# Kernel optimization log

Measured on AMD Instinct MI355X. Metric: run time of the kernel, lower is better.

The kernel has to match this reference:

```python
import jax, jax.numpy as jnp
import numpy as np

B, S, H, L, NH, F, V, K, R = 64, 512, 256, 4, 8, 1024, 50265, 8, 25
DH = H // NH
EPS = 1e-5


def layernorm(x, g, b):
    mu = x.mean(-1, keepdims=True)
    var = ((x - mu) ** 2).mean(-1, keepdims=True)
    return (x - mu) * jax.lax.rsqrt(var + EPS) * g + b


def setup_inputs() -> dict:
    key = jax.random.key(0)
    ks = jax.random.split(key, 24)
    input_ids = jax.random.randint(ks[0], (B, S), 0, V, dtype=jnp.int64)
    # prefix attention mask with variable valid lengths (ragged sequences)
    lengths = jax.random.randint(ks[1], (B,), 16, S + 1)
    attention_mask = (jnp.arange(S)[None, :] < lengths[:, None]).astype(jnp.int32)
    sub_indices = jax.random.randint(ks[2], (B, K), 0, S, dtype=jnp.int64)
    obj_indices = jax.random.randint(ks[3], (B, K), 0, S, dtype=jnp.int64)
    sub_counts = jax.random.randint(ks[4], (B,), 0, K + 1, dtype=jnp.int32)
    obj_counts = jax.random.randint(ks[5], (B,), 0, K + 1, dtype=jnp.int32)
    sc = 0.02
    p = {
        'emb': jax.random.normal(ks[6], (V, H), jnp.float32) * sc,
        'Wqkv': jax.random.normal(ks[7], (L, H, 3 * H), jnp.float32) * sc,
        'bqkv': jnp.zeros((L, 3 * H), jnp.float32),
        'Wo': jax.random.normal(ks[8], (L, H, H), jnp.float32) * sc,
        'bo': jnp.zeros((L, H), jnp.float32),
        'ln1_g': jnp.ones((L, H), jnp.float32), 'ln1_b': jnp.zeros((L, H), jnp.float32),
        'ln2_g': jnp.ones((L, H), jnp.float32), 'ln2_b': jnp.zeros((L, H), jnp.float32),
        'W1': jax.random.normal(ks[9], (L, H, F), jnp.float32) * sc,
        'b1': jnp.zeros((L, F), jnp.float32),
        'W2': jax.random.normal(ks[10], (L, F, H), jnp.float32) * sc,
        'b2': jnp.zeros((L, H), jnp.float32),
        'lnf_g': jnp.ones((H,), jnp.float32), 'lnf_b': jnp.zeros((H,), jnp.float32),
        'mW1': jax.random.normal(ks[11], (3 * H, H), jnp.float32) * sc,
        'mb1': jnp.zeros((H,), jnp.float32),
        'mW2': jax.random.normal(ks[12], (H, R), jnp.float32) * sc,
        'mb2': jnp.zeros((R,), jnp.float32),
    }
    return dict(input_ids=input_ids, attention_mask=attention_mask,
                sub_indices=sub_indices, sub_counts=sub_counts,
                obj_indices=obj_indices, obj_counts=obj_counts, **p)


def _encoder(input_ids, attention_mask, emb, Wqkv, bqkv, Wo, bo,
             ln1_g, ln1_b, ln2_g, ln2_b, W1, b1, W2, b2, lnf_g, lnf_b):
    x = emb[input_ids]  # [B,S,H]
    kbias = jnp.where(attention_mask[:, None, None, :] > 0, 0.0, -1e9)  # mask keys
    scale = 1.0 / np.sqrt(DH)
    for l in range(L):  # small fixed layer loop
        qkv = x @ Wqkv[l] + bqkv[l]
        q, k, v = jnp.split(qkv, 3, axis=-1)
        q = q.reshape(B, S, NH, DH).transpose(0, 2, 1, 3)
        k = k.reshape(B, S, NH, DH).transpose(0, 2, 1, 3)
        v = v.reshape(B, S, NH, DH).transpose(0, 2, 1, 3)
        scores = jnp.einsum('bhqd,bhkd->bhqk', q, k) * scale + kbias
        attn = jax.nn.softmax(scores, axis=-1)
        o = jnp.einsum('bhqk,bhkd->bhqd', attn, v).transpose(0, 2, 1, 3).reshape(B, S, H)
        x = layernorm(x + o @ Wo[l] + bo[l], ln1_g[l], ln1_b[l])
        h = jax.nn.relu(x @ W1[l] + b1[l]) @ W2[l] + b2[l]
        x = layernorm(x + h, ln2_g[l], ln2_b[l])
    return layernorm(x, lnf_g, lnf_b)


def _pooled(seq, idx, counts):
    g = jnp.take_along_axis(seq, idx[:, :, None], axis=1)  # [B,K,H]
    m = (jnp.arange(K)[None, :] < counts[:, None]).astype(seq.dtype)
    s = (g * m[:, :, None]).sum(1)
    c = counts.astype(seq.dtype)[:, None]
    return jnp.where(c > 0, s / jnp.maximum(c, 1.0), 0.0)  # zeros if no indices


def reference(input_ids, attention_mask, sub_indices, sub_counts, obj_indices, obj_counts,
              emb, Wqkv, bqkv, Wo, bo, ln1_g, ln1_b, ln2_g, ln2_b,
              W1, b1, W2, b2, lnf_g, lnf_b, mW1, mb1, mW2, mb2):
    seq = _encoder(input_ids, attention_mask, emb, Wqkv, bqkv, Wo, bo,
                   ln1_g, ln1_b, ln2_g, ln2_b, W1, b1, W2, b2, lnf_g, lnf_b)
    sub = _pooled(seq, sub_indices, sub_counts)
    obj = _pooled(seq, obj_indices, obj_counts)
    mask = attention_mask.astype(seq.dtype)
    lens = mask.sum(1)[:, None]
    story = jnp.where(lens > 0, (seq * mask[:, :, None]).sum(1) / jnp.maximum(lens, 1.0),
                      seq.mean(1))
    feat = jnp.concatenate([sub, obj, story], axis=-1)  # [B,3H]
    logits = jax.nn.relu(feat @ mW1 + mb1) @ mW2 + mb2
    return logits
```

## Files before the change

kernel.cpp:

```cpp
#include <hip/hip_runtime.h>
#include <hip/hip_bf16.h>


typedef __hip_bfloat16 bf16;
typedef __attribute__((ext_vector_type(8))) short short8;
typedef __attribute__((ext_vector_type(4))) float f32x4;

#define S_LEN 512
#define H_DIM 256
#define NTOK  32768
#define QSCALE 0.25503488f

__device__ __forceinline__ void gload_lds16(const void* g, void* l) {
  __builtin_amdgcn_global_load_lds(
      (const __attribute__((address_space(1))) unsigned int*)g,
      (__attribute__((address_space(3))) unsigned int*)l, 16, 0, 0);
}

__device__ __forceinline__ unsigned short f2bu(float x) {
  bf16 t = __float2bfloat16(x);
  return *reinterpret_cast<unsigned short*>(&t);
}

__global__ __launch_bounds__(64) void lens_kernel(
    const int* __restrict__ amask, int* __restrict__ ntiles,
    int* __restrict__ lenb) {
  const int b = blockIdx.x, t = threadIdx.x;
  int c = 0;
#pragma unroll
  for (int i = 0; i < 8; ++i) c += amask[b * S_LEN + t + i * 64];
#pragma unroll
  for (int off = 1; off < 64; off <<= 1) c += __shfl_xor(c, off);
  if (t == 0) {
    lenb[b] = c;
    ntiles[b] = (c + 63) >> 6;
  }
}

__global__ __launch_bounds__(64) void order_kernel(
    const int* __restrict__ ntiles, int* __restrict__ ordb) {
  const int b = threadIdx.x;
  const int ntb = ntiles[b];
  int rank = 0;
  for (int j = 0; j < 64; ++j) {
    const int ntj = __shfl(ntb, j);
    rank += (ntj > ntb) || (ntj == ntb && j < b);
  }
  ordb[rank] = b;
}

__global__ __launch_bounds__(256) void tcast_kernel(
    const float* __restrict__ in, bf16* __restrict__ out, int K, int N) {
  const int l = blockIdx.z;
  in  += (size_t)l * K * N;
  out += (size_t)l * K * N;
  __shared__ float t[32][33];
  const int n0 = blockIdx.x * 32, k0 = blockIdx.y * 32;
  const int c = threadIdx.x & 31, r = threadIdx.x >> 5;
#pragma unroll
  for (int rr = r; rr < 32; rr += 8)
    t[rr][c] = in[(size_t)(k0 + rr) * N + n0 + c];
  __syncthreads();
#pragma unroll
  for (int rr = r; rr < 32; rr += 8)
    out[(size_t)(n0 + rr) * K + k0 + c] = __float2bfloat16(t[c][rr]);
}

__global__ __launch_bounds__(256) void embed_kernel(
    const int* __restrict__ ids, const float* __restrict__ emb,
    float* __restrict__ X, bf16* __restrict__ Xb) {
  size_t i4 = (size_t)blockIdx.x * 256 + threadIdx.x;
  int tok = (int)(i4 >> 6);
  int d4  = (int)(i4 & 63);
  float4 v = *(const float4*)&emb[(size_t)ids[tok] * H_DIM + d4 * 4];
  *(float4*)&X[i4 * 4] = v;
  ushort4 pk;
  pk.x = f2bu(v.x); pk.y = f2bu(v.y); pk.z = f2bu(v.z); pk.w = f2bu(v.w);
  *(ushort4*)&Xb[i4 * 4] = pk;
}

#define SRC_CHUNK(tid_) (((tid_) & 3) ^ (((tid_) >> 3) & 3))

template<int MODE, bool RELU>
__global__ __launch_bounds__(256) void hgemm_kernel(
    const bf16* __restrict__ A, const bf16* __restrict__ Bt,
    const float* __restrict__ bias, float* __restrict__ Cf,
    bf16* __restrict__ Cb, bf16* __restrict__ Vt,
    int M, int N, int K) {
  __shared__ __align__(16) bf16 Sh[16384];
  bf16* const As0 = Sh;
  bf16* const Bs0 = Sh + 8192;
  const int tid = threadIdx.x;
  const int wv = tid >> 6, ln = tid & 63;
  const int fr = ln & 15, g4 = ln >> 4;
  const int wr = wv >> 1, wc = wv & 1;
  const int m0 = blockIdx.x * 128, n0 = blockIdx.y * 128;
  const int lr = tid >> 2;
  const int lk = SRC_CHUNK(tid) * 8;
  const int rc = (g4 ^ ((fr >> 1) & 3)) * 8;

#define STAGE_G(buf, kk) do {                                                  \
    const int kof_ = (kk) * 32;                                                \
    gload_lds16(A  + (size_t)(m0 + lr) * K + kof_ + lk,                        \
                &As0[(buf) * 4096 + wv * 512]);                                \
    gload_lds16(A  + (size_t)(m0 + 64 + lr) * K + kof_ + lk,                   \
                &As0[(buf) * 4096 + 2048 + wv * 512]);                         \
    gload_lds16(Bt + (size_t)(n0 + lr) * K + kof_ + lk,                        \
                &Bs0[(buf) * 4096 + wv * 512]);                                \
    gload_lds16(Bt + (size_t)(n0 + 64 + lr) * K + kof_ + lk,                   \
                &Bs0[(buf) * 4096 + 2048 + wv * 512]);                         \
  } while (0)

  f32x4 acc[4][4];
#pragma unroll
  for (int i = 0; i < 4; ++i)
#pragma unroll
    for (int j = 0; j < 4; ++j)
      acc[i][j] = (f32x4){0.f, 0.f, 0.f, 0.f};

  const int NT = K >> 5;
  STAGE_G(0, 0);
  __syncthreads();
  int cur = 0;
  for (int kt = 0; kt < NT; ++kt) {
    if (kt + 1 < NT) STAGE_G(cur ^ 1, kt + 1);
    short8 af[4], bfv[4];
#pragma unroll
    for (int i = 0; i < 4; ++i)
      af[i] = *(const short8*)
          &As0[cur * 4096 + (wr * 64 + i * 16 + fr) * 32 + rc];
#pragma unroll
    for (int j = 0; j < 4; ++j)
      bfv[j] = *(const short8*)
          &Bs0[cur * 4096 + (wc * 64 + j * 16 + fr) * 32 + rc];
#pragma unroll
    for (int i = 0; i < 4; ++i)
#pragma unroll
      for (int j = 0; j < 4; ++j)
        acc[i][j] = __builtin_amdgcn_mfma_f32_16x16x32_bf16(
            af[i], bfv[j], acc[i][j], 0, 0, 0);
    __syncthreads();
    cur ^= 1;
  }
#undef STAGE_G

  const bool vpath = (MODE == 2) && (n0 >= 512);
#pragma unroll
  for (int j = 0; j < 4; ++j) {
    const int nl = wc * 64 + j * 16 + fr;
    const int n = n0 + nl;
    const float bv = bias[n];
    const float sc = (MODE == 2 && n < 256) ? QSCALE : 1.0f;
#pragma unroll
    for (int i = 0; i < 4; ++i) {
      const int mlb = wr * 64 + i * 16 + g4 * 4;
#pragma unroll
      for (int r = 0; r < 4; ++r) {
        float o = acc[i][j][r] + bv;
        if (RELU) o = fmaxf(o, 0.f);
        o *= sc;
        const int ml = mlb + r;
        const int addr = vpath ? nl * 128 + (ml ^ ((nl & 7) << 3))
                               : ml * 128 + (nl ^ ((ml & 7) << 3));
        Sh[addr] = __float2bfloat16(o);
      }
    }
  }
  __syncthreads();
  if (!vpath) {
    const int ldc = (MODE == 1) ? N : 768;
#pragma unroll
    for (int p = 0; p < 8; ++p) {
      const int cid = p * 256 + tid;
      const int ml = cid >> 4, mc = cid & 15;
      const short8 v =
          *(const short8*)&Sh[ml * 128 + ((mc * 8) ^ ((ml & 7) << 3))];
      *(short8*)&Cb[(size_t)(m0 + ml) * ldc + n0 + mc * 8] = v;
    }
  } else {
    const int bb = m0 >> 9;
#pragma unroll
    for (int p = 0; p < 8; ++p) {
      const int cid = p * 256 + tid;
      const int ddl = cid >> 4, mc = cid & 15;
      const short8 v =
          *(const short8*)&Sh[ddl * 128 + ((mc * 8) ^ ((ddl & 7) << 3))];
      const int dd = (n0 - 512) + ddl;
      const int hh = dd >> 5, ddd = dd & 31;
      const int s8 = (m0 & 511) + mc * 8;
      const int ssw = (s8 & ~63) | ((s8 & 63) ^ ((ddd & 7) << 3));
      *(short8*)&Vt[(((size_t)bb * 8 + hh) * 32 + ddd) * 512 + ssw] = v;
    }
  }
}

__global__ __launch_bounds__(256) void hgemm_ln_kernel(
    const bf16* __restrict__ A, const bf16* __restrict__ Bt,
    const float* __restrict__ bias, float* __restrict__ X,
    bf16* __restrict__ Xb, const float* __restrict__ g,
    const float* __restrict__ bt, int K) {
  __shared__ __align__(16) bf16 Sh[20480];
  bf16* const As0 = Sh;
  bf16* const Bs0 = Sh + 4096;
  float* const rsum = (float*)Sh;
  float* const rsq  = (float*)(Sh + 512);
  bf16*  const XbT  = Sh + 1024;
  float* const XfT  = (float*)(Sh + 1024);
  const int tid = threadIdx.x;
  const int wv = tid >> 6;
  const int ln = tid & 63;
  const int fr = ln & 15, g4 = ln >> 4;
  const int m0 = blockIdx.x * 64;
  const int rc = (g4 ^ ((fr >> 1) & 3)) * 8;

#define STAGE_L(buf, kk) do {                                                  \
    const int kof_ = (kk) * 32;                                                \
    gload_lds16(A + (size_t)(m0 + (tid >> 2)) * K + kof_ +                     \
                    SRC_CHUNK(tid) * 8,                                        \
                &As0[(buf) * 2048 + wv * 512]);                                \
    _Pragma("unroll")                                                          \
    for (int e = 0; e < 4; ++e) {                                              \
      const int vt = e * 256 + tid;                                            \
      gload_lds16(Bt + (size_t)(vt >> 2) * K + kof_ + SRC_CHUNK(vt) * 8,       \
                  &Bs0[(buf) * 8192 + e * 2048 + wv * 512]);                   \
    }                                                                          \
  } while (0)

  f32x4 acc[4][4];
#pragma unroll
  for (int i = 0; i < 4; ++i)
#pragma unroll
    for (int j = 0; j < 4; ++j)
      acc[i][j] = (f32x4){0.f, 0.f, 0.f, 0.f};

  const int NT = K >> 5;
  STAGE_L(0, 0);
  __syncthreads();
  int cur = 0;
  for (int kt = 0; kt < NT; ++kt) {
    if (kt + 1 < NT) STAGE_L(cur ^ 1, kt + 1);
    short8 af[4], bfv[4];
#pragma unroll
    for (int i = 0; i < 4; ++i)
      af[i] = *(const short8*)&As0[cur * 2048 + (i * 16 + fr) * 32 + rc];
#pragma unroll
    for (int j = 0; j < 4; ++j)
      bfv[j] = *(const short8*)
          &Bs0[cur * 8192 + (wv * 64 + j * 16 + fr) * 32 + rc];
#pragma unroll
    for (int i = 0; i < 4; ++i)
#pragma unroll
      for (int j = 0; j < 4; ++j)
        acc[i][j] = __builtin_amdgcn_mfma_f32_16x16x32_bf16(
            af[i], bfv[j], acc[i][j], 0, 0, 0);
    __syncthreads();
    cur ^= 1;
  }
#undef STAGE_L

  float gj[4], bj[4], bsj[4];
#pragma unroll
  for (int j = 0; j < 4; ++j) {
    const int n = wv * 64 + j * 16 + fr;
    gj[j] = g[n]; bj[j] = bt[n]; bsj[j] = bias[n];
  }
#pragma unroll
  for (int i = 0; i < 4; ++i) {
#pragma unroll
    for (int r = 0; r < 4; ++r) {
      const int m = m0 + i * 16 + g4 * 4 + r;
#pragma unroll
      for (int j = 0; j < 4; ++j)
        acc[i][j][r] += bsj[j] + X[(size_t)m * 256 + wv * 64 + j * 16 + fr];
    }
  }
#pragma unroll
  for (int i = 0; i < 4; ++i) {
#pragma unroll
    for (int r = 0; r < 4; ++r) {
      float sp = acc[i][0][r] + acc[i][1][r] + acc[i][2][r] + acc[i][3][r];
      float qp = acc[i][0][r] * acc[i][0][r] + acc[i][1][r] * acc[i][1][r] +
                 acc[i][2][r] * acc[i][2][r] + acc[i][3][r] * acc[i][3][r];
#pragma unroll
      for (int off = 1; off < 16; off <<= 1) {
        sp += __shfl_xor(sp, off);
        qp += __shfl_xor(qp, off);
      }
      if (fr == 0) {
        const int ri = i * 16 + g4 * 4 + r;
        rsum[wv * 64 + ri] = sp;
        rsq[wv * 64 + ri] = qp;
      }
    }
  }
  __syncthreads();
#pragma unroll
  for (int i = 0; i < 4; ++i) {
#pragma unroll
    for (int r = 0; r < 4; ++r) {
      const int ri = i * 16 + g4 * 4 + r;
      const float tot = rsum[ri] + rsum[64 + ri] + rsum[128 + ri] +
                        rsum[192 + ri];
      const float tq = rsq[ri] + rsq[64 + ri] + rsq[128 + ri] + rsq[192 + ri];
      const float mu = tot * (1.0f / 256.0f);
      const float var = tq * (1.0f / 256.0f) - mu * mu;
      const float rstd = rsqrtf(var + 1e-5f);
#pragma unroll
      for (int j = 0; j < 4; ++j)
        acc[i][j][r] = (acc[i][j][r] - mu) * rstd * gj[j] + bj[j];
    }
  }
  __syncthreads();
#pragma unroll
  for (int i = 0; i < 4; ++i)
#pragma unroll
    for (int r = 0; r < 4; ++r) {
      const int ml = i * 16 + g4 * 4 + r;
#pragma unroll
      for (int j = 0; j < 4; ++j) {
        const int nl = wv * 64 + j * 16 + fr;
        XbT[ml * 256 + (nl ^ ((ml & 7) << 3))] = __float2bfloat16(acc[i][j][r]);
      }
    }
  __syncthreads();
#pragma unroll
  for (int p = 0; p < 8; ++p) {
    const int c8 = p * 256 + tid;
    const int row = c8 >> 5, cc = c8 & 31;
    const short8 v =
        *(const short8*)&XbT[row * 256 + ((cc * 8) ^ ((row & 7) << 3))];
    *(short8*)&Xb[(size_t)(m0 + row) * 256 + cc * 8] = v;
  }
#pragma unroll
  for (int pass = 0; pass < 2; ++pass) {
    __syncthreads();
    if ((wv >> 1) == pass) {
      const int cbase = (wv & 1) * 64;
#pragma unroll
      for (int i = 0; i < 4; ++i)
#pragma unroll
        for (int r = 0; r < 4; ++r) {
          const int ml = i * 16 + g4 * 4 + r;
#pragma unroll
          for (int j = 0; j < 4; ++j) {
            const int c = cbase + j * 16 + fr;
            XfT[ml * 128 + (c ^ ((ml & 7) << 2))] = acc[i][j][r];
          }
        }
    }
    __syncthreads();
#pragma unroll
    for (int p = 0; p < 8; ++p) {
      const int c4 = p * 256 + tid;
      const int row = c4 >> 5, cc = c4 & 31;
      const float4 v = *(const float4*)
          &XfT[row * 128 + ((cc * 4) ^ ((row & 7) << 2))];
      *(float4*)&X[(size_t)(m0 + row) * 256 + pass * 128 + cc * 4] = v;
    }
  }
}

__global__ __launch_bounds__(256) void attn_mfma_kernel(
    const bf16* __restrict__ QKVb, const bf16* __restrict__ Vt,
    const int* __restrict__ amask, const int* __restrict__ ntiles,
    const int* __restrict__ ordb, bf16* __restrict__ Ob) {
  const int b = ordb[blockIdx.z];
  const int h = blockIdx.y, q0 = blockIdx.x * 64;
  const int tid = threadIdx.x;
  const int wv = tid >> 6, ln = tid & 63;
  const int fr = ln & 15, g4 = ln >> 4;
  const int f8 = (fr & 7) << 3;
  const int rc = (g4 ^ ((fr >> 1) & 3)) * 8;
  const int bh32 = (b * 8 + h) * 32;
  __shared__ __align__(16) bf16 Ks[2][2048];
  __shared__ __align__(16) bf16 Vs[2][2048];
  __shared__ __align__(16) bf16 Ps[4096];
  __shared__ __align__(16) float Ms[64];

  const int nt = ntiles[b];

#define STAGE_A(buf, kt_) do {                                                 \
    const int k0_ = (kt_) * 64;                                                \
    gload_lds16(QKVb + (size_t)(b * S_LEN + k0_ + (tid >> 2)) * 768 + 256 +    \
                    h * 32 + SRC_CHUNK(tid) * 8,                               \
                &Ks[(buf)][wv * 512]);                                         \
    gload_lds16(Vt + (size_t)(bh32 + (tid >> 3)) * 512 + k0_ + (tid & 7) * 8,  \
                &Vs[(buf)][wv * 512]);                                         \
    if ((kt_) == nt - 1 && tid < 64)                                           \
      Ms[tid] = (amask[b * S_LEN + k0_ + tid] != 0) ? 0.f : -1e9f;             \
  } while (0)

  gload_lds16(QKVb + (size_t)(b * S_LEN + q0 + (tid >> 2)) * 768 + h * 32 +
                  SRC_CHUNK(tid) * 8,
              &Ps[wv * 512]);
  STAGE_A(0, 0);
  __syncthreads();
  const short8 qb = *(const short8*)&Ps[(wv * 16 + fr) * 32 + rc];
  __syncthreads();

  f32x4 accO[2];
  accO[0] = (f32x4){0.f, 0.f, 0.f, 0.f};
  accO[1] = (f32x4){0.f, 0.f, 0.f, 0.f};
  float mrun = -1e30f, lrun = 0.f;
  const int srcq = 20 * g4;

  int cur = 0;
  for (int kt = 0; kt < nt; ++kt) {
    if (kt + 1 < nt) STAGE_A(cur ^ 1, kt + 1);
    const bool bnd = (kt == nt - 1);

    f32x4 st[4];
#pragma unroll
    for (int kb = 0; kb < 4; ++kb) {
      const short8 kf = *(const short8*)&Ks[cur][(kb * 16 + fr) * 32 + rc];
      f32x4 z = (f32x4){0.f, 0.f, 0.f, 0.f};
      st[kb] = __builtin_amdgcn_mfma_f32_16x16x32_bf16(kf, qb, z, 0, 0, 0);
    }

    float p[16];
    if (bnd) {
#pragma unroll
      for (int kb = 0; kb < 4; ++kb) {
        const f32x4 mv = ((const f32x4*)Ms)[kb * 4 + g4];
#pragma unroll
        for (int rr = 0; rr < 4; ++rr) p[kb * 4 + rr] = st[kb][rr] + mv[rr];
      }
    } else {
#pragma unroll
      for (int kb = 0; kb < 4; ++kb)
#pragma unroll
        for (int rr = 0; rr < 4; ++rr) p[kb * 4 + rr] = st[kb][rr];
    }

    const float a0 = fmaxf(fmaxf(p[0], p[1]), p[2]);
    const float a1 = fmaxf(fmaxf(p[3], p[4]), p[5]);
    const float a2 = fmaxf(fmaxf(p[6], p[7]), p[8]);
    const float a3 = fmaxf(fmaxf(p[9], p[10]), p[11]);
    const float a4 = fmaxf(fmaxf(p[12], p[13]), p[14]);
    float mx = fmaxf(fmaxf(fmaxf(a0, a1), fmaxf(a2, a3)), fmaxf(a4, p[15]));
    mx = fmaxf(mx, __shfl_xor(mx, 16));
    mx = fmaxf(mx, __shfl_xor(mx, 32));

    float corr = 1.f;
    if (!__all(mx <= mrun + 8.f)) {
      const float mnew = fmaxf(mrun, mx);
      corr = exp2f(mrun - mnew);
      mrun = mnew;
#pragma unroll
      for (int rr = 0; rr < 4; ++rr) {
        const float cs = __shfl(corr, srcq + rr);
        accO[0][rr] *= cs;
        accO[1][rr] *= cs;
      }
    }

#pragma unroll
    for (int i = 0; i < 16; ++i) p[i] = exp2f(p[i] - mrun);
    const float b0 = p[0] + p[1], b1 = p[2] + p[3], b2 = p[4] + p[5],
                b3 = p[6] + p[7], b4 = p[8] + p[9], b5 = p[10] + p[11],
                b6 = p[12] + p[13], b7 = p[14] + p[15];
    float ps = ((b0 + b1) + (b2 + b3)) + ((b4 + b5) + (b6 + b7));
    ps += __shfl_xor(ps, 16);
    ps += __shfl_xor(ps, 32);
    lrun = lrun * corr + ps;

#pragma unroll
    for (int kb = 0; kb < 4; ++kb) {
      ushort4 w4;
      w4.x = f2bu(p[kb * 4 + 0]);
      w4.y = f2bu(p[kb * 4 + 1]);
      w4.z = f2bu(p[kb * 4 + 2]);
      w4.w = f2bu(p[kb * 4 + 3]);
      *(ushort4*)&Ps[wv * 1024 + fr * 64 + ((kb * 16 + g4 * 4) ^ f8)] = w4;
    }

#pragma unroll
    for (int kk = 0; kk < 2; ++kk) {
      const short8 pa = *(const short8*)
          &Ps[wv * 1024 + fr * 64 + ((kk * 32 + g4 * 8) ^ f8)];
#pragma unroll
      for (int df = 0; df < 2; ++df) {
        const short8 vb = *(const short8*)
            &Vs[cur][(df * 16 + fr) * 64 + ((kk * 32 + g4 * 8) ^ f8)];
        accO[df] = __builtin_amdgcn_mfma_f32_16x16x32_bf16(
            pa, vb, accO[df], 0, 0, 0);
      }
    }
    __syncthreads();
    cur ^= 1;
  }
#undef STAGE_A

  const float inv = 1.0f / lrun;
#pragma unroll
  for (int rr = 0; rr < 4; ++rr) {
    const float iv = __shfl(inv, srcq + rr);
    const int q = q0 + wv * 16 + g4 * 4 + rr;
    const size_t orow = ((size_t)b * S_LEN + q) * H_DIM + h * 32;
    Ob[orow + fr]      = __float2bfloat16(accO[0][rr] * iv);
    Ob[orow + 16 + fr] = __float2bfloat16(accO[1][rr] * iv);
  }
}

__global__ __launch_bounds__(256) void lnf_pool_kernel(
    float* __restrict__ X, const float* __restrict__ g,
    const float* __restrict__ bt, const int* __restrict__ amask,
    float* __restrict__ Pstory) {
  const int b = blockIdx.x, sg = blockIdx.y;
  const int tid = threadIdx.x, wv = tid >> 6, ln = tid & 63;
  const float4 gg = ((const float4*)g)[ln];
  const float4 bb = ((const float4*)bt)[ln];
  float ax = 0.f, ay = 0.f, az = 0.f, aw = 0.f;
  for (int t = wv; t < 64; t += 4) {
    const size_t tok = (size_t)b * S_LEN + sg * 64 + t;
    float4 v = ((const float4*)X)[tok * 64 + ln];
    float s = v.x + v.y + v.z + v.w;
#pragma unroll
    for (int off = 1; off < 64; off <<= 1) s += __shfl_xor(s, off);
    const float mu = s * (1.0f / 256.0f);
    const float dx = v.x - mu, dy = v.y - mu, dz = v.z - mu, dw = v.w - mu;
    float sq = dx * dx + dy * dy + dz * dz + dw * dw;
#pragma unroll
    for (int off = 1; off < 64; off <<= 1) sq += __shfl_xor(sq, off);
    const float rstd = rsqrtf(sq * (1.0f / 256.0f) + 1e-5f);
    float4 o;
    o.x = dx * rstd * gg.x + bb.x;
    o.y = dy * rstd * gg.y + bb.y;
    o.z = dz * rstd * gg.z + bb.z;
    o.w = dw * rstd * gg.w + bb.w;
    ((float4*)X)[tok * 64 + ln] = o;
    if (amask[tok]) { ax += o.x; ay += o.y; az += o.z; aw += o.w; }
  }
  __shared__ float part[4][256];
  part[wv][ln * 4 + 0] = ax;
  part[wv][ln * 4 + 1] = ay;
  part[wv][ln * 4 + 2] = az;
  part[wv][ln * 4 + 3] = aw;
  __syncthreads();
  const float tot = part[0][tid] + part[1][tid] + part[2][tid] + part[3][tid];
  Pstory[((size_t)b * 8 + sg) * 256 + tid] = tot;
}

__global__ __launch_bounds__(256) void poolcls_kernel(
    const float* __restrict__ X, const float* __restrict__ Pstory,
    const int* __restrict__ lenb,
    const int* __restrict__ sub_idx, const int* __restrict__ sub_cnt,
    const int* __restrict__ obj_idx, const int* __restrict__ obj_cnt,
    const float* __restrict__ mW1, const float* __restrict__ mb1,
    const float* __restrict__ mW2, const float* __restrict__ mb2,
    float* __restrict__ out) {
  const int b = blockIdx.x, t = threadIdx.x;
  __shared__ float fs[768];
  __shared__ float hid[256];
  const float* xb = X + (size_t)b * S_LEN * H_DIM;
  {
    float s = 0.f;
#pragma unroll
    for (int i = 0; i < 8; ++i) s += Pstory[((size_t)b * 8 + i) * 256 + t];
    fs[512 + t] = s / (float)lenb[b];
  }
  {
    const int cc = sub_cnt[b];
    float s2 = 0.f;
    for (int j = 0; j < cc; ++j)
      s2 += xb[(size_t)sub_idx[b * 8 + j] * H_DIM + t];
    fs[t] = (cc > 0) ? s2 / (float)cc : 0.f;
  }
  {
    const int cc = obj_cnt[b];
    float s2 = 0.f;
    for (int j = 0; j < cc; ++j)
      s2 += xb[(size_t)obj_idx[b * 8 + j] * H_DIM + t];
    fs[256 + t] = (cc > 0) ? s2 / (float)cc : 0.f;
  }
  __syncthreads();
  float acc = mb1[t];
  for (int k = 0; k < 768; ++k) acc += fs[k] * mW1[(size_t)k * 256 + t];
  hid[t] = fmaxf(acc, 0.f);
  __syncthreads();
  if (t < 25) {
    float o = mb2[t];
    for (int j = 0; j < 256; ++j) o += hid[j] * mW2[j * 25 + t];
    out[b * 25 + t] = o;
  }
}

extern "C" void kernel_launch(void* const* d_in, const int* in_sizes, int n_in,
                              void* d_out, int out_size, void* d_ws, size_t ws_size,
                              hipStream_t stream) {
  const int*   input_ids = (const int*)d_in[0];
  const int*   amask     = (const int*)d_in[1];
  const int*   sub_idx   = (const int*)d_in[2];
  const int*   sub_cnt   = (const int*)d_in[3];
  const int*   obj_idx   = (const int*)d_in[4];
  const int*   obj_cnt   = (const int*)d_in[5];
  const float* emb  = (const float*)d_in[6];
  const float* Wqkv = (const float*)d_in[7];
  const float* bqkv = (const float*)d_in[8];
  const float* Wo   = (const float*)d_in[9];
  const float* bo   = (const float*)d_in[10];
  const float* ln1g = (const float*)d_in[11];
  const float* ln1b = (const float*)d_in[12];
  const float* ln2g = (const float*)d_in[13];
  const float* ln2b = (const float*)d_in[14];
  const float* W1   = (const float*)d_in[15];
  const float* b1   = (const float*)d_in[16];
  const float* W2   = (const float*)d_in[17];
  const float* b2   = (const float*)d_in[18];
  const float* lnfg = (const float*)d_in[19];
  const float* lnfb = (const float*)d_in[20];
  const float* mW1  = (const float*)d_in[21];
  const float* mb1  = (const float*)d_in[22];
  const float* mW2  = (const float*)d_in[23];
  const float* mb2  = (const float*)d_in[24];
  float* out = (float*)d_out;

  char* w = (char*)d_ws;
  float* X    = (float*)w;                         w += (size_t)NTOK * 256 * 4;
  bf16*  Xb   = (bf16*)w;                          w += (size_t)NTOK * 256 * 2;
  bf16*  QKVb = (bf16*)w;                          w += (size_t)NTOK * 768 * 2;
  bf16*  Vtg  = (bf16*)w;                          w += (size_t)NTOK * 256 * 2;
  bf16*  Ob   = (bf16*)w;                          w += (size_t)NTOK * 256 * 2;
  bf16*  Wqkvt= (bf16*)w;                          w += (size_t)4 * 768 * 256 * 2;
  bf16*  Wot  = (bf16*)w;                          w += (size_t)4 * 256 * 256 * 2;
  bf16*  W1t  = (bf16*)w;                          w += (size_t)4 * 1024 * 256 * 2;
  bf16*  W2t  = (bf16*)w;                          w += (size_t)4 * 256 * 1024 * 2;
  float* Pstory = (float*)w;                       w += (size_t)64 * 8 * 256 * 4;
  int*   ntiles = (int*)w;                         w += 256;
  int*   lenb   = (int*)w;                         w += 256;
  int*   ordb   = (int*)w;                         w += 256;
  bf16*  Hb   = QKVb;

  lens_kernel<<<64, 64, 0, stream>>>(amask, ntiles, lenb);
  order_kernel<<<1, 64, 0, stream>>>(ntiles, ordb);
  tcast_kernel<<<dim3(24, 8, 4), 256, 0, stream>>>(Wqkv, Wqkvt, 256, 768);
  tcast_kernel<<<dim3(8, 8, 4), 256, 0, stream>>>(Wo, Wot, 256, 256);
  tcast_kernel<<<dim3(32, 8, 4), 256, 0, stream>>>(W1, W1t, 256, 1024);
  tcast_kernel<<<dim3(8, 32, 4), 256, 0, stream>>>(W2, W2t, 1024, 256);

  embed_kernel<<<8192, 256, 0, stream>>>(input_ids, emb, X, Xb);

  for (int l = 0; l < 4; ++l) {
    const bf16* Wqkvt_l = Wqkvt + (size_t)l * 768 * 256;
    const bf16* Wot_l   = Wot + (size_t)l * 256 * 256;
    const bf16* W1t_l   = W1t + (size_t)l * 1024 * 256;
    const bf16* W2t_l   = W2t + (size_t)l * 256 * 1024;

    hgemm_kernel<2, false><<<dim3(256, 6), 256, 0, stream>>>(
        Xb, Wqkvt_l, bqkv + (size_t)l * 768, nullptr, QKVb, Vtg, NTOK, 768, 256);
    attn_mfma_kernel<<<dim3(8, 8, 64), 256, 0, stream>>>(
        QKVb, Vtg, amask, ntiles, ordb, Ob);
    hgemm_ln_kernel<<<512, 256, 0, stream>>>(
        Ob, Wot_l, bo + (size_t)l * 256, X, Xb,
        ln1g + l * 256, ln1b + l * 256, 256);
    hgemm_kernel<1, true><<<dim3(256, 8), 256, 0, stream>>>(
        Xb, W1t_l, b1 + (size_t)l * 1024, nullptr, Hb, nullptr, NTOK, 1024, 256);
    hgemm_ln_kernel<<<512, 256, 0, stream>>>(
        Hb, W2t_l, b2 + (size_t)l * 256, X, Xb,
        ln2g + l * 256, ln2b + l * 256, 1024);
  }
  lnf_pool_kernel<<<dim3(64, 8), 256, 0, stream>>>(X, lnfg, lnfb, amask, Pstory);
  poolcls_kernel<<<64, 256, 0, stream>>>(X, Pstory, lenb, sub_idx, sub_cnt,
                                         obj_idx, obj_cnt, mW1, mb1, mW2, mb2,
                                         out);
}
```

Measured before the change: 730.0 us.

## Keep residual stream in bf16 only and compute softmax row sums via MFMA

```diff
diff --git a/kernel.cpp b/kernel.cpp
--- a/kernel.cpp
+++ b/kernel.cpp
@@ -20,6 +20,10 @@
 __device__ __forceinline__ unsigned short f2bu(float x) {
   bf16 t = __float2bfloat16(x);
   return *reinterpret_cast<unsigned short*>(&t);
+}
+__device__ __forceinline__ float bu2f(unsigned short u) {
+  unsigned int x = (unsigned int)u << 16;
+  return __uint_as_float(x);
 }
 
 __global__ __launch_bounds__(64) void lens_kernel(
@@ -68,12 +72,11 @@
 
 __global__ __launch_bounds__(256) void embed_kernel(
     const int* __restrict__ ids, const float* __restrict__ emb,
-    float* __restrict__ X, bf16* __restrict__ Xb) {
+    bf16* __restrict__ Xb) {
   size_t i4 = (size_t)blockIdx.x * 256 + threadIdx.x;
   int tok = (int)(i4 >> 6);
   int d4  = (int)(i4 & 63);
   float4 v = *(const float4*)&emb[(size_t)ids[tok] * H_DIM + d4 * 4];
-  *(float4*)&X[i4 * 4] = v;
   ushort4 pk;
   pk.x = f2bu(v.x); pk.y = f2bu(v.y); pk.z = f2bu(v.z); pk.w = f2bu(v.w);
   *(ushort4*)&Xb[i4 * 4] = pk;
@@ -196,16 +199,14 @@
 
 __global__ __launch_bounds__(256) void hgemm_ln_kernel(
     const bf16* __restrict__ A, const bf16* __restrict__ Bt,
-    const float* __restrict__ bias, float* __restrict__ X,
-    bf16* __restrict__ Xb, const float* __restrict__ g,
-    const float* __restrict__ bt, int K) {
+    const float* __restrict__ bias, bf16* __restrict__ Xbf,
+    const float* __restrict__ g, const float* __restrict__ bt, int K) {
   __shared__ __align__(16) bf16 Sh[20480];
   bf16* const As0 = Sh;
   bf16* const Bs0 = Sh + 4096;
   float* const rsum = (float*)Sh;
   float* const rsq  = (float*)(Sh + 512);
   bf16*  const XbT  = Sh + 1024;
-  float* const XfT  = (float*)(Sh + 1024);
   const int tid = threadIdx.x;
   const int wv = tid >> 6;
   const int ln = tid & 63;
@@ -258,6 +259,15 @@
   }
 #undef STAGE_L
 
+#pragma unroll
+  for (int p = 0; p < 8; ++p) {
+    const int seg = p * 4 + wv;
+    gload_lds16(Xbf + (size_t)(m0 + seg * 2 + (ln >> 5)) * 256 +
+                    (ln & 31) * 8,
+                &XbT[seg * 512]);
+  }
+  __syncthreads();
+
   float gj[4], bj[4], bsj[4];
 #pragma unroll
   for (int j = 0; j < 4; ++j) {
@@ -268,10 +278,13 @@
   for (int i = 0; i < 4; ++i) {
 #pragma unroll
     for (int r = 0; r < 4; ++r) {
-      const int m = m0 + i * 16 + g4 * 4 + r;
-#pragma unroll
-      for (int j = 0; j < 4; ++j)
-        acc[i][j][r] += bsj[j] + X[(size_t)m * 256 + wv * 64 + j * 16 + fr];
+      const int ml = i * 16 + g4 * 4 + r;
+#pragma unroll
+      for (int j = 0; j < 4; ++j) {
+        const int nl = wv * 64 + j * 16 + fr;
+        acc[i][j][r] += bsj[j] +
+            bu2f(*(const unsigned short*)&XbT[ml * 256 + nl]);
+      }
     }
   }
 #pragma unroll
@@ -306,22 +319,13 @@
       const float var = tq * (1.0f / 256.0f) - mu * mu;
       const float rstd = rsqrtf(var + 1e-5f);
 #pragma unroll
-      for (int j = 0; j < 4; ++j)
-        acc[i][j][r] = (acc[i][j][r] - mu) * rstd * gj[j] + bj[j];
-    }
-  }
-  __syncthreads();
-#pragma unroll
-  for (int i = 0; i < 4; ++i)
-#pragma unroll
-    for (int r = 0; r < 4; ++r) {
-      const int ml = i * 16 + g4 * 4 + r;
-#pragma unroll
       for (int j = 0; j < 4; ++j) {
         const int nl = wv * 64 + j * 16 + fr;
-        XbT[ml * 256 + (nl ^ ((ml & 7) << 3))] = __float2bfloat16(acc[i][j][r]);
-      }
-    }
+        const float o = (acc[i][j][r] - mu) * rstd * gj[j] + bj[j];
+        XbT[ri * 256 + (nl ^ ((ri & 7) << 3))] = __float2bfloat16(o);
+      }
+    }
+  }
   __syncthreads();
 #pragma unroll
   for (int p = 0; p < 8; ++p) {
@@ -329,34 +333,7 @@
     const int row = c8 >> 5, cc = c8 & 31;
     const short8 v =
         *(const short8*)&XbT[row * 256 + ((cc * 8) ^ ((row & 7) << 3))];
-    *(short8*)&Xb[(size_t)(m0 + row) * 256 + cc * 8] = v;
-  }
-#pragma unroll
-  for (int pass = 0; pass < 2; ++pass) {
-    __syncthreads();
-    if ((wv >> 1) == pass) {
-      const int cbase = (wv & 1) * 64;
-#pragma unroll
-      for (int i = 0; i < 4; ++i)
-#pragma unroll
-        for (int r = 0; r < 4; ++r) {
-          const int ml = i * 16 + g4 * 4 + r;
-#pragma unroll
-          for (int j = 0; j < 4; ++j) {
-            const int c = cbase + j * 16 + fr;
-            XfT[ml * 128 + (c ^ ((ml & 7) << 2))] = acc[i][j][r];
-          }
-        }
-    }
-    __syncthreads();
-#pragma unroll
-    for (int p = 0; p < 8; ++p) {
-      const int c4 = p * 256 + tid;
-      const int row = c4 >> 5, cc = c4 & 31;
-      const float4 v = *(const float4*)
-          &XfT[row * 128 + ((cc * 4) ^ ((row & 7) << 2))];
-      *(float4*)&X[(size_t)(m0 + row) * 256 + pass * 128 + cc * 4] = v;
-    }
+    *(short8*)&Xbf[(size_t)(m0 + row) * 256 + cc * 8] = v;
   }
 }
 
@@ -398,10 +375,14 @@
   const short8 qb = *(const short8*)&Ps[(wv * 16 + fr) * 32 + rc];
   __syncthreads();
 
-  f32x4 accO[2];
+  f32x4 accO[2], accS;
   accO[0] = (f32x4){0.f, 0.f, 0.f, 0.f};
   accO[1] = (f32x4){0.f, 0.f, 0.f, 0.f};
-  float mrun = -1e30f, lrun = 0.f;
+  accS    = (f32x4){0.f, 0.f, 0.f, 0.f};
+  short8 ones;
+#pragma unroll
+  for (int z = 0; z < 8; ++z) ones[z] = (short)0x3F80;
+  float mrun = -1e30f;
   const int srcq = 20 * g4;
 
   int cur = 0;
@@ -441,28 +422,21 @@
     mx = fmaxf(mx, __shfl_xor(mx, 16));
     mx = fmaxf(mx, __shfl_xor(mx, 32));
 
-    float corr = 1.f;
     if (!__all(mx <= mrun + 8.f)) {
       const float mnew = fmaxf(mrun, mx);
-      corr = exp2f(mrun - mnew);
+      const float corr = exp2f(mrun - mnew);
       mrun = mnew;
 #pragma unroll
       for (int rr = 0; rr < 4; ++rr) {
         const float cs = __shfl(corr, srcq + rr);
         accO[0][rr] *= cs;
         accO[1][rr] *= cs;
+        accS[rr]    *= cs;
       }
     }
 
 #pragma unroll
     for (int i = 0; i < 16; ++i) p[i] = exp2f(p[i] - mrun);
-    const float b0 = p[0] + p[1], b1 = p[2] + p[3], b2 = p[4] + p[5],
-                b3 = p[6] + p[7], b4 = p[8] + p[9], b5 = p[10] + p[11],
-                b6 = p[12] + p[13], b7 = p[14] + p[15];
-    float ps = ((b0 + b1) + (b2 + b3)) + ((b4 + b5) + (b6 + b7));
-    ps += __shfl_xor(ps, 16);
-    ps += __shfl_xor(ps, 32);
-    lrun = lrun * corr + ps;
 
 #pragma unroll
     for (int kb = 0; kb < 4; ++kb) {
@@ -478,6 +452,7 @@
     for (int kk = 0; kk < 2; ++kk) {
       const short8 pa = *(const short8*)
           &Ps[wv * 1024 + fr * 64 + ((kk * 32 + g4 * 8) ^ f8)];
+      accS = __builtin_amdgcn_mfma_f32_16x16x32_bf16(pa, ones, accS, 0, 0, 0);
 #pragma unroll
       for (int df = 0; df < 2; ++df) {
         const short8 vb = *(const short8*)
@@ -491,10 +466,9 @@
   }
 #undef STAGE_A
 
-  const float inv = 1.0f / lrun;
 #pragma unroll
   for (int rr = 0; rr < 4; ++rr) {
-    const float iv = __shfl(inv, srcq + rr);
+    const float iv = 1.0f / accS[rr];
     const int q = q0 + wv * 16 + g4 * 4 + rr;
     const size_t orow = ((size_t)b * S_LEN + q) * H_DIM + h * 32;
     Ob[orow + fr]      = __float2bfloat16(accO[0][rr] * iv);
@@ -503,7 +477,7 @@
 }
 
 __global__ __launch_bounds__(256) void lnf_pool_kernel(
-    float* __restrict__ X, const float* __restrict__ g,
+    bf16* __restrict__ Xbf, const float* __restrict__ g,
     const float* __restrict__ bt, const int* __restrict__ amask,
     float* __restrict__ Pstory) {
   const int b = blockIdx.x, sg = blockIdx.y;
@@ -513,23 +487,26 @@
   float ax = 0.f, ay = 0.f, az = 0.f, aw = 0.f;
   for (int t = wv; t < 64; t += 4) {
     const size_t tok = (size_t)b * S_LEN + sg * 64 + t;
-    float4 v = ((const float4*)X)[tok * 64 + ln];
-    float s = v.x + v.y + v.z + v.w;
+    const ushort4 u = *(const ushort4*)&Xbf[tok * 256 + ln * 4];
+    const float vx = bu2f(u.x), vy = bu2f(u.y), vz = bu2f(u.z),
+                vw = bu2f(u.w);
+    float s = vx + vy + vz + vw;
 #pragma unroll
     for (int off = 1; off < 64; off <<= 1) s += __shfl_xor(s, off);
     const float mu = s * (1.0f / 256.0f);
-    const float dx = v.x - mu, dy = v.y - mu, dz = v.z - mu, dw = v.w - mu;
+    const float dx = vx - mu, dy = vy - mu, dz = vz - mu, dw = vw - mu;
     float sq = dx * dx + dy * dy + dz * dz + dw * dw;
 #pragma unroll
     for (int off = 1; off < 64; off <<= 1) sq += __shfl_xor(sq, off);
     const float rstd = rsqrtf(sq * (1.0f / 256.0f) + 1e-5f);
-    float4 o;
-    o.x = dx * rstd * gg.x + bb.x;
-    o.y = dy * rstd * gg.y + bb.y;
-    o.z = dz * rstd * gg.z + bb.z;
-    o.w = dw * rstd * gg.w + bb.w;
-    ((float4*)X)[tok * 64 + ln] = o;
-    if (amask[tok]) { ax += o.x; ay += o.y; az += o.z; aw += o.w; }
+    const float ox = dx * rstd * gg.x + bb.x;
+    const float oy = dy * rstd * gg.y + bb.y;
+    const float oz = dz * rstd * gg.z + bb.z;
+    const float ow = dw * rstd * gg.w + bb.w;
+    ushort4 o4;
+    o4.x = f2bu(ox); o4.y = f2bu(oy); o4.z = f2bu(oz); o4.w = f2bu(ow);
+    *(ushort4*)&Xbf[tok * 256 + ln * 4] = o4;
+    if (amask[tok]) { ax += ox; ay += oy; az += oz; aw += ow; }
   }
   __shared__ float part[4][256];
   part[wv][ln * 4 + 0] = ax;
@@ -542,7 +519,7 @@
 }
 
 __global__ __launch_bounds__(256) void poolcls_kernel(
-    const float* __restrict__ X, const float* __restrict__ Pstory,
+    const bf16* __restrict__ Xbf, const float* __restrict__ Pstory,
     const int* __restrict__ lenb,
     const int* __restrict__ sub_idx, const int* __restrict__ sub_cnt,
     const int* __restrict__ obj_idx, const int* __restrict__ obj_cnt,
@@ -552,7 +529,7 @@
   const int b = blockIdx.x, t = threadIdx.x;
   __shared__ float fs[768];
   __shared__ float hid[256];
-  const float* xb = X + (size_t)b * S_LEN * H_DIM;
+  const bf16* xb = Xbf + (size_t)b * S_LEN * H_DIM;
   {
     float s = 0.f;
 #pragma unroll
@@ -563,14 +540,14 @@
     const int cc = sub_cnt[b];
     float s2 = 0.f;
     for (int j = 0; j < cc; ++j)
-      s2 += xb[(size_t)sub_idx[b * 8 + j] * H_DIM + t];
+      s2 += __bfloat162float(xb[(size_t)sub_idx[b * 8 + j] * H_DIM + t]);
     fs[t] = (cc > 0) ? s2 / (float)cc : 0.f;
   }
   {
     const int cc = obj_cnt[b];
     float s2 = 0.f;
     for (int j = 0; j < cc; ++j)
-      s2 += xb[(size_t)obj_idx[b * 8 + j] * H_DIM + t];
+      s2 += __bfloat162float(xb[(size_t)obj_idx[b * 8 + j] * H_DIM + t]);
     fs[256 + t] = (cc > 0) ? s2 / (float)cc : 0.f;
   }
   __syncthreads();
@@ -616,7 +593,6 @@
   float* out = (float*)d_out;
 
   char* w = (char*)d_ws;
-  float* X    = (float*)w;                         w += (size_t)NTOK * 256 * 4;
   bf16*  Xb   = (bf16*)w;                          w += (size_t)NTOK * 256 * 2;
   bf16*  QKVb = (bf16*)w;                          w += (size_t)NTOK * 768 * 2;
   bf16*  Vtg  = (bf16*)w;                          w += (size_t)NTOK * 256 * 2;
@@ -638,7 +614,7 @@
   tcast_kernel<<<dim3(32, 8, 4), 256, 0, stream>>>(W1, W1t, 256, 1024);
   tcast_kernel<<<dim3(8, 32, 4), 256, 0, stream>>>(W2, W2t, 1024, 256);
 
-  embed_kernel<<<8192, 256, 0, stream>>>(input_ids, emb, X, Xb);
+  embed_kernel<<<8192, 256, 0, stream>>>(input_ids, emb, Xb);
 
   for (int l = 0; l < 4; ++l) {
     const bf16* Wqkvt_l = Wqkvt + (size_t)l * 768 * 256;
@@ -651,16 +627,17 @@
     attn_mfma_kernel<<<dim3(8, 8, 64), 256, 0, stream>>>(
         QKVb, Vtg, amask, ntiles, ordb, Ob);
     hgemm_ln_kernel<<<512, 256, 0, stream>>>(
-        Ob, Wot_l, bo + (size_t)l * 256, X, Xb,
+        Ob, Wot_l, bo + (size_t)l * 256, Xb,
         ln1g + l * 256, ln1b + l * 256, 256);
     hgemm_kernel<1, true><<<dim3(256, 8), 256, 0, stream>>>(
         Xb, W1t_l, b1 + (size_t)l * 1024, nullptr, Hb, nullptr, NTOK, 1024, 256);
     hgemm_ln_kernel<<<512, 256, 0, stream>>>(
-        Hb, W2t_l, b2 + (size_t)l * 256, X, Xb,
+        Hb, W2t_l, b2 + (size_t)l * 256, Xb,
         ln2g + l * 256, ln2b + l * 256, 1024);
   }
-  lnf_pool_kernel<<<dim3(64, 8), 256, 0, stream>>>(X, lnfg, lnfb, amask, Pstory);
-  poolcls_kernel<<<64, 256, 0, stream>>>(X, Pstory, lenb, sub_idx, sub_cnt,
+  lnf_pool_kernel<<<dim3(64, 8), 256, 0, stream>>>(Xb, lnfg, lnfb, amask,
+                                                   Pstory);
+  poolcls_kernel<<<64, 256, 0, stream>>>(Xb, Pstory, lenb, sub_idx, sub_cnt,
                                          obj_idx, obj_cnt, mW1, mb1, mW2, mb2,
                                          out);
 }
```

After: 705.5 us. 3.4% less time.
